# Performance work log

Hardware: AMD Instinct MI355X
Metric: run time of the kernel (lower is better)

Reference implementation:

```python
import jax, jax.numpy as jnp
import numpy as np

CONF_THR = 0.2      # confidence_threshold default
NMS_THR = 0.45      # nms_threshold default
TARGET_ID = 0       # NAME2ID['person'] in COCO ordering
CLASS_OFFSET = 1e4  # per-class box offset so cross-class IoU == 0 (per-class NMS)
B, N, C = 4, 8192, 80


def setup_inputs() -> dict:
    key = jax.random.key(0)
    kxy, kwh, kobj, kcls = jax.random.split(key, 4)
    xy = jax.random.uniform(kxy, (B, N, 2)) * 600.0          # x1, y1
    wh = jax.random.uniform(kwh, (B, N, 2)) * 100.0 + 1.0    # box w, h
    boxes = jnp.concatenate([xy, xy + wh], axis=-1)           # x1 y1 x2 y2
    obj = jax.random.uniform(kobj, (B, N, 1))                 # objectness score
    clsp = jax.random.uniform(kcls, (B, N, C))                # class probs
    detection = jnp.concatenate([boxes, obj, clsp], axis=-1)  # [B, N, 5+C]
    return {"detection": detection}


def _pairwise_iou(b):
    # b: [N, 4] in x1y1x2y2
    area = (b[:, 2] - b[:, 0]) * (b[:, 3] - b[:, 1])
    lt = jnp.maximum(b[:, None, :2], b[None, :, :2])
    rb = jnp.minimum(b[:, None, 2:], b[None, :, 2:])
    wh = jnp.clip(rb - lt, 0.0)
    inter = wh[..., 0] * wh[..., 1]
    return inter / (area[:, None] + area[None, :] - inter + 1e-9)


def _nms_image(boxes, scores, classprobs, labels):
    # Fixed-shape, masked equivalent of the torch per-image filter+per-class NMS.
    valid = (scores > CONF_THR) & (labels == TARGET_ID)
    s = jnp.where(valid, scores, -1.0)
    order = jnp.argsort(-s)  # descending score (NMS visiting order)
    b = boxes[order]
    s = s[order]
    cp = classprobs[order]
    lb = labels[order]
    v = valid[order]
    # Offset boxes per class label -> IoU between different classes is 0,
    # which exactly reproduces the per-class NMS loop.
    ob = b + lb.astype(b.dtype)[:, None] * CLASS_OFFSET
    iou = _pairwise_iou(ob)  # [N, N]

    def step(keep, xs):
        row, i, vi = xs
        suppressed = jnp.any(keep & (row > NMS_THR))
        k = vi & jnp.logical_not(suppressed)
        return keep.at[i].set(k), k

    _, keep = jax.lax.scan(
        step, jnp.zeros(s.shape[0], dtype=bool), (iou, jnp.arange(s.shape[0]), v)
    )
    # Compact kept detections to the front (stable sort preserves descending score
    # order among kept boxes, matching the final argsort in torch).
    s_rank = jnp.where(keep, s, -1.0)
    final = jnp.argsort(-s_rank)
    kf = keep[final]
    m = kf.astype(b.dtype)
    out_boxes = b[final] * m[:, None]
    out_scores = jnp.where(kf, s[final], 0.0)
    out_classprobs = cp[final] * m
    out_labels = jnp.where(kf, lb[final], -1)
    return out_boxes, out_scores, out_classprobs, out_labels


def reference(detection):
    # split_detections
    boxes = detection[..., :4]           # [B, N, 4]
    scores = detection[..., 4]           # [B, N]
    cls = detection[..., 5:]             # [B, N, C]
    classprobs = jnp.max(cls, axis=-1)
    labels = jnp.argmax(cls, axis=-1)
    # filter_detections, batched over images
    return jax.vmap(_nms_image)(boxes, scores, classprobs, labels)
```

## Files before the change

### kernel.cpp

```cpp
#include <hip/hip_runtime.h>
#include <cstdint>
#include <cstddef>

typedef unsigned long long u64;

#define BB 4
#define NN 8192
#define DSTRIDE 85
#define RPB 64
#define BPI 128
#define NBLK (BB * BPI)
#define RCAP 64
#define SCAP 192
#define CONF_THRF 0.2f
#define NMS_THRF 0.45f
#define PLANE (BB * NN)
#define IMSZ 16640
#define MARK 0x5EED

__device__ __forceinline__ void wave_fence() {
  __asm__ volatile("" ::: "memory");
  __builtin_amdgcn_wave_barrier();
  __asm__ volatile("" ::: "memory");
}

__global__ __launch_bounds__(256) void fused_kernel(
    const float* __restrict__ det, float* __restrict__ out,
    int* __restrict__ counts, float* __restrict__ cand) {
  __shared__ __align__(16) char arena[4 * IMSZ];
  __shared__ int wcnt[4];
  const int tid = threadIdx.x;
  const int blk = blockIdx.x;
  const int wave = tid >> 6, lane = tid & 63;

  {
    const float4* src =
        reinterpret_cast<const float4*>(det + (size_t)blk * (RPB * DSTRIDE));
    float4* dst = reinterpret_cast<float4*>(arena);
    for (int i = tid; i < (RPB * DSTRIDE) / 4; i += 256) dst[i] = src[i];
  }
  __syncthreads();

  const float* st = reinterpret_cast<const float*>(arena);
  const int r = tid >> 2, q = tid & 3;
  float best = -1.0f; int barg = 0;
  {
    const float* rowp = st + r * DSTRIDE + 5 + 20 * q;
#pragma unroll
    for (int k = 0; k < 20; ++k) {
      float v = rowp[k];
      if (v > best) { best = v; barg = 20 * q + k; }
    }
  }
#pragma unroll
  for (int off = 1; off <= 2; off <<= 1) {
    float ov = __shfl_xor(best, off);
    int oa = __shfl_xor(barg, off);
    if (ov > best || (ov == best && oa < barg)) { best = ov; barg = oa; }
  }
  float4 box = make_float4(0.f, 0.f, 0.f, 0.f);
  float score = 0.f;
  bool valid = false;
  if (q == 0) {
    const float* rp = st + r * DSTRIDE;
    box = make_float4(rp[0], rp[1], rp[2], rp[3]);
    score = rp[4];
    valid = (score > CONF_THRF) && (barg == 0);
  }
  const int base = blk * RPB;
  if (tid < 64) {
    reinterpret_cast<float4*>(out)[base + tid] = make_float4(0.f, 0.f, 0.f, 0.f);
  } else if (tid < 128) {
    out[(size_t)PLANE * 4 + base + (tid - 64)] = 0.f;
  } else if (tid < 192) {
    out[(size_t)PLANE * 5 + base + (tid - 128)] = 0.f;
  } else {
    out[(size_t)PLANE * 6 + base + (tid - 192)] = -1.0f;
  }
  u64 mask = __ballot(valid);
  if (lane == 0) wcnt[wave] = __popcll(mask);
  __syncthreads();
  int bcount = wcnt[0] + wcnt[1] + wcnt[2] + wcnt[3];
  if (valid) {
    int offw = (wave > 0 ? wcnt[0] : 0) + (wave > 1 ? wcnt[1] : 0) +
               (wave > 2 ? wcnt[2] : 0);
    int pos = __popcll(mask & ((1ull << lane) - 1ull));
    float4* p =
        reinterpret_cast<float4*>(cand + ((size_t)blk * RCAP + offw + pos) * 8);
    p[0] = box;
    p[1] = make_float4(score, best,
                       __int_as_float((blk & (BPI - 1)) * RPB + r), 0.f);
  }
  __syncthreads();
  if (tid == 0)
    __hip_atomic_store(&counts[blk], (MARK << 16) | bcount, __ATOMIC_RELEASE,
                       __HIP_MEMORY_SCOPE_AGENT);

  if (blk != NBLK - 1) return;

  const int img = wave;
  char* A = arena + img * IMSZ;
  u64* keys = reinterpret_cast<u64*>(A);
  u64* mat = reinterpret_cast<u64*>(A + 1536);
  float* ux1 = reinterpret_cast<float*>(A + 6144);
  float* uy1 = reinterpret_cast<float*>(A + 6912);
  float* ux2 = reinterpret_cast<float*>(A + 7680);
  float* uy2 = reinterpret_cast<float*>(A + 8448);
  float* usc = reinterpret_cast<float*>(A + 9216);
  float* ucp = reinterpret_cast<float*>(A + 9984);
  float* sx1 = reinterpret_cast<float*>(A + 10752);
  float* sy1 = reinterpret_cast<float*>(A + 11520);
  float* sx2 = reinterpret_cast<float*>(A + 12288);
  float* sy2 = reinterpret_cast<float*>(A + 13056);
  float* sar = reinterpret_cast<float*>(A + 13824);
  float* ssc = reinterpret_cast<float*>(A + 14592);
  float* scp = reinterpret_cast<float*>(A + 15360);

  const int m0 = img * BPI + lane, m1 = m0 + 64;
  int v0, v1;
  do {
    v0 = __hip_atomic_load(&counts[m0], __ATOMIC_ACQUIRE,
                           __HIP_MEMORY_SCOPE_AGENT);
  } while ((v0 >> 16) != MARK);
  do {
    v1 = __hip_atomic_load(&counts[m1], __ATOMIC_ACQUIRE,
                           __HIP_MEMORY_SCOPE_AGENT);
  } while ((v1 >> 16) != MARK);
  int c0 = v0 & 0xFFFF, c1 = v1 & 0xFFFF;

  int s0 = c0;
#pragma unroll
  for (int d = 1; d < 64; d <<= 1) {
    int t = __shfl_up(s0, d);
    if (lane >= d) s0 += t;
  }
  int tot0 = __shfl(s0, 63);
  int s1 = c1;
#pragma unroll
  for (int d = 1; d < 64; d <<= 1) {
    int t = __shfl_up(s1, d);
    if (lane >= d) s1 += t;
  }
  s1 += tot0;
  int K = __shfl(s1, 63);
  if (K > SCAP) K = SCAP;
  int e0 = s0 - c0, e1 = s1 - c1;

#pragma unroll
  for (int pass = 0; pass < 2; ++pass) {
    int m = pass ? m1 : m0;
    int c = pass ? c1 : c0;
    int e = pass ? e1 : e0;
    const float4* p = reinterpret_cast<const float4*>(cand + (size_t)m * RCAP * 8);
    for (int k = 0; k < c; ++k) {
      int o = e + k;
      if (o < SCAP) {
        float4 a = p[2 * k], bq = p[2 * k + 1];
        ux1[o] = a.x; uy1[o] = a.y; ux2[o] = a.z; uy2[o] = a.w;
        usc[o] = bq.x; ucp[o] = bq.y;
        int idx = __float_as_int(bq.z);
        keys[o] = ((u64)__float_as_uint(bq.x) << 32) |
                  ((u64)(unsigned)(0xFFFF - idx) << 16) | (unsigned)o;
      }
    }
  }
  wave_fence();

  for (int o = lane; o < K; o += 64) {
    u64 my = keys[o];
    int rr = 0;
    for (int s = 0; s < K; ++s) rr += (keys[s] > my) ? 1 : 0;
    float x1 = ux1[o], y1 = uy1[o], x2 = ux2[o], y2 = uy2[o];
    sx1[rr] = x1; sy1[rr] = y1; sx2[rr] = x2; sy2[rr] = y2;
    sar[rr] = (x2 - x1) * (y2 - y1);
    ssc[rr] = usc[o]; scp[rr] = ucp[o];
  }
  wave_fence();

  for (int i = lane; i < K; i += 64) {
    float ax1 = sx1[i], ay1 = sy1[i], ax2 = sx2[i], ay2 = sy2[i], aa = sar[i];
    u64 w0 = 0, w1 = 0, w2 = 0;
    for (int j = i + 1; j < K; ++j) {
      float xx1 = fmaxf(ax1, sx1[j]);
      float yy1 = fmaxf(ay1, sy1[j]);
      float xx2 = fminf(ax2, sx2[j]);
      float yy2 = fminf(ay2, sy2[j]);
      float w = fmaxf(xx2 - xx1, 0.f);
      float h = fmaxf(yy2 - yy1, 0.f);
      float inter = w * h;
      float iou = inter / (aa + sar[j] - inter + 1e-9f);
      if (iou > NMS_THRF) {
        u64 bit = 1ull << (j & 63);
        int wj = j >> 6;
        w0 |= (wj == 0) ? bit : 0;
        w1 |= (wj == 1) ? bit : 0;
        w2 |= (wj == 2) ? bit : 0;
      }
    }
    mat[i * 3] = w0; mat[i * 3 + 1] = w1; mat[i * 3 + 2] = w2;
  }
  wave_fence();

  u64 rem0 = 0, rem1 = 0, rem2 = 0, kp0 = 0, kp1 = 0, kp2 = 0;
#define GREEDY_CHUNK(WW, REMW, KPW)                                      \
  for (int ii = 0; ii < 64; ++ii) {                                      \
    int i = (WW) * 64 + ii;                                              \
    if (i >= K) break;                                                   \
    u64 g0 = mat[i * 3], g1 = mat[i * 3 + 1], g2 = mat[i * 3 + 2];       \
    if (!((REMW >> ii) & 1ull)) {                                        \
      KPW |= 1ull << ii;                                                 \
      rem0 |= g0; rem1 |= g1; rem2 |= g2;                                \
    }                                                                    \
  }
  GREEDY_CHUNK(0, rem0, kp0)
  GREEDY_CHUNK(1, rem1, kp1)
  GREEDY_CHUNK(2, rem2, kp2)
#undef GREEDY_CHUNK

  for (int i = lane; i < K; i += 64) {
    int wi = i >> 6, bi = i & 63;
    u64 kw = (wi == 0) ? kp0 : (wi == 1) ? kp1 : kp2;
    if ((kw >> bi) & 1ull) {
      int rr = (wi > 0 ? __popcll(kp0) : 0) + (wi > 1 ? __popcll(kp1) : 0) +
               __popcll(kw & ((1ull << bi) - 1ull));
      size_t o = (size_t)img * NN + rr;
      reinterpret_cast<float4*>(out)[o] =
          make_float4(sx1[i], sy1[i], sx2[i], sy2[i]);
      out[(size_t)PLANE * 4 + o] = ssc[i];
      out[(size_t)PLANE * 5 + o] = scp[i];
      out[(size_t)PLANE * 6 + o] = 0.0f;
    }
  }
}

extern "C" void kernel_launch(void* const* d_in, const int* in_sizes, int n_in,
                              void* d_out, int out_size, void* d_ws, size_t ws_size,
                              hipStream_t stream) {
  const float* det = (const float*)d_in[0];
  float* out = (float*)d_out;
  int* counts = (int*)d_ws;
  float* cand = (float*)((char*)d_ws + 2048);

  fused_kernel<<<NBLK, 256, 0, stream>>>(det, out, counts, cand);
}
```

Measured before the change: 97.01 us.

## Split fused kernel into scan and per-image NMS kernels

```diff
diff --git a/kernel.cpp b/kernel.cpp
--- a/kernel.cpp
+++ b/kernel.cpp
@@ -15,58 +15,49 @@
 #define CONF_THRF 0.2f
 #define NMS_THRF 0.45f
 #define PLANE (BB * NN)
-#define IMSZ 16640
-#define MARK 0x5EED
 
 __device__ __forceinline__ void wave_fence() {
-  __asm__ volatile("" ::: "memory");
+  __asm__ volatile("s_waitcnt lgkmcnt(0)" ::: "memory");
   __builtin_amdgcn_wave_barrier();
-  __asm__ volatile("" ::: "memory");
-}
-
-__global__ __launch_bounds__(256) void fused_kernel(
+}
+
+__global__ __launch_bounds__(256) void scan_kernel(
     const float* __restrict__ det, float* __restrict__ out,
     int* __restrict__ counts, float* __restrict__ cand) {
-  __shared__ __align__(16) char arena[4 * IMSZ];
   __shared__ int wcnt[4];
   const int tid = threadIdx.x;
   const int blk = blockIdx.x;
-  const int wave = tid >> 6, lane = tid & 63;
-
-  {
-    const float4* src =
-        reinterpret_cast<const float4*>(det + (size_t)blk * (RPB * DSTRIDE));
-    float4* dst = reinterpret_cast<float4*>(arena);
-    for (int i = tid; i < (RPB * DSTRIDE) / 4; i += 256) dst[i] = src[i];
-  }
-  __syncthreads();
-
-  const float* st = reinterpret_cast<const float*>(arena);
   const int r = tid >> 2, q = tid & 3;
+  const int row = blk * RPB + r;
+  const float* d = det + (size_t)row * DSTRIDE;
+
   float best = -1.0f; int barg = 0;
-  {
-    const float* rowp = st + r * DSTRIDE + 5 + 20 * q;
-#pragma unroll
-    for (int k = 0; k < 20; ++k) {
-      float v = rowp[k];
-      if (v > best) { best = v; barg = 20 * q + k; }
-    }
+  const float* cb = d + 5 + 20 * q;
+#pragma unroll
+  for (int k = 0; k < 5; ++k) {
+    float4 v = *reinterpret_cast<const float4*>(cb + 4 * k);
+    int c0 = 20 * q + 4 * k;
+    if (v.x > best) { best = v.x; barg = c0; }
+    if (v.y > best) { best = v.y; barg = c0 + 1; }
+    if (v.z > best) { best = v.z; barg = c0 + 2; }
+    if (v.w > best) { best = v.w; barg = c0 + 3; }
   }
 #pragma unroll
   for (int off = 1; off <= 2; off <<= 1) {
     float ov = __shfl_xor(best, off);
-    int oa = __shfl_xor(barg, off);
+    int   oa = __shfl_xor(barg, off);
     if (ov > best || (ov == best && oa < barg)) { best = ov; barg = oa; }
   }
+
   float4 box = make_float4(0.f, 0.f, 0.f, 0.f);
   float score = 0.f;
   bool valid = false;
   if (q == 0) {
-    const float* rp = st + r * DSTRIDE;
-    box = make_float4(rp[0], rp[1], rp[2], rp[3]);
-    score = rp[4];
+    box = *reinterpret_cast<const float4*>(d);
+    score = d[4];
     valid = (score > CONF_THRF) && (barg == 0);
   }
+
   const int base = blk * RPB;
   if (tid < 64) {
     reinterpret_cast<float4*>(out)[base + tid] = make_float4(0.f, 0.f, 0.f, 0.f);
@@ -77,56 +68,39 @@
   } else {
     out[(size_t)PLANE * 6 + base + (tid - 192)] = -1.0f;
   }
+
   u64 mask = __ballot(valid);
+  const int wave = tid >> 6, lane = tid & 63;
   if (lane == 0) wcnt[wave] = __popcll(mask);
   __syncthreads();
-  int bcount = wcnt[0] + wcnt[1] + wcnt[2] + wcnt[3];
   if (valid) {
     int offw = (wave > 0 ? wcnt[0] : 0) + (wave > 1 ? wcnt[1] : 0) +
                (wave > 2 ? wcnt[2] : 0);
     int pos = __popcll(mask & ((1ull << lane) - 1ull));
-    float4* p =
-        reinterpret_cast<float4*>(cand + ((size_t)blk * RCAP + offw + pos) * 8);
-    p[0] = box;
-    p[1] = make_float4(score, best,
-                       __int_as_float((blk & (BPI - 1)) * RPB + r), 0.f);
-  }
-  __syncthreads();
-  if (tid == 0)
-    __hip_atomic_store(&counts[blk], (MARK << 16) | bcount, __ATOMIC_RELEASE,
-                       __HIP_MEMORY_SCOPE_AGENT);
-
-  if (blk != NBLK - 1) return;
-
-  const int img = wave;
-  char* A = arena + img * IMSZ;
-  u64* keys = reinterpret_cast<u64*>(A);
-  u64* mat = reinterpret_cast<u64*>(A + 1536);
-  float* ux1 = reinterpret_cast<float*>(A + 6144);
-  float* uy1 = reinterpret_cast<float*>(A + 6912);
-  float* ux2 = reinterpret_cast<float*>(A + 7680);
-  float* uy2 = reinterpret_cast<float*>(A + 8448);
-  float* usc = reinterpret_cast<float*>(A + 9216);
-  float* ucp = reinterpret_cast<float*>(A + 9984);
-  float* sx1 = reinterpret_cast<float*>(A + 10752);
-  float* sy1 = reinterpret_cast<float*>(A + 11520);
-  float* sx2 = reinterpret_cast<float*>(A + 12288);
-  float* sy2 = reinterpret_cast<float*>(A + 13056);
-  float* sar = reinterpret_cast<float*>(A + 13824);
-  float* ssc = reinterpret_cast<float*>(A + 14592);
-  float* scp = reinterpret_cast<float*>(A + 15360);
+    float* p = cand + ((size_t)blk * RCAP + (offw + pos)) * 8;
+    reinterpret_cast<float4*>(p)[0] = box;
+    reinterpret_cast<float4*>(p)[1] =
+        make_float4(score, best, __int_as_float(row & (NN - 1)), 0.f);
+  }
+  if (tid == 0) counts[blk] = wcnt[0] + wcnt[1] + wcnt[2] + wcnt[3];
+}
+
+__global__ __launch_bounds__(64) void nms_kernel(
+    float* __restrict__ out, const int* __restrict__ counts,
+    const float* __restrict__ cand) {
+  __shared__ u64 keys[SCAP];
+  __shared__ u64 mat[SCAP * 3];
+  __shared__ float ux1[SCAP], uy1[SCAP], ux2[SCAP], uy2[SCAP];
+  __shared__ float usc[SCAP], ucp[SCAP];
+  __shared__ float sx1[SCAP], sy1[SCAP], sx2[SCAP], sy2[SCAP];
+  __shared__ float sar[SCAP], ssc[SCAP], scp[SCAP];
+
+  const int img = blockIdx.x;
+  const int lane = threadIdx.x;
 
   const int m0 = img * BPI + lane, m1 = m0 + 64;
-  int v0, v1;
-  do {
-    v0 = __hip_atomic_load(&counts[m0], __ATOMIC_ACQUIRE,
-                           __HIP_MEMORY_SCOPE_AGENT);
-  } while ((v0 >> 16) != MARK);
-  do {
-    v1 = __hip_atomic_load(&counts[m1], __ATOMIC_ACQUIRE,
-                           __HIP_MEMORY_SCOPE_AGENT);
-  } while ((v1 >> 16) != MARK);
-  int c0 = v0 & 0xFFFF, c1 = v1 & 0xFFFF;
+  int c0 = counts[m0];
+  int c1 = counts[m1];
 
   int s0 = c0;
 #pragma unroll
@@ -151,7 +125,8 @@
     int m = pass ? m1 : m0;
     int c = pass ? c1 : c0;
     int e = pass ? e1 : e0;
-    const float4* p = reinterpret_cast<const float4*>(cand + (size_t)m * RCAP * 8);
+    const float4* p =
+        reinterpret_cast<const float4*>(cand + (size_t)m * RCAP * 8);
     for (int k = 0; k < c; ++k) {
       int o = e + k;
       if (o < SCAP) {
@@ -241,5 +216,6 @@
   int* counts = (int*)d_ws;
   float* cand = (float*)((char*)d_ws + 2048);
 
-  fused_kernel<<<NBLK, 256, 0, stream>>>(det, out, counts, cand);
-}
+  scan_kernel<<<NBLK, 256, 0, stream>>>(det, out, counts, cand);
+  nms_kernel<<<BB, 64, 0, stream>>>(out, counts, cand);
+}
```

Measured after the change: 87.12 us. 10.2% less time.
